# Optimization experiments

Measured on AMD Instinct MI355X. Metric: run time of the kernel, lower is better.

## Reference

```python
import jax, jax.numpy as jnp
import numpy as np

N_STATE = 1024
N_HEAD = 16
HEAD_DIM = N_STATE // N_HEAD


def setup_inputs() -> dict:
    key = jax.random.key(0)
    ks = jax.random.split(key, 8)
    s = 0.02
    return {
        "x": jax.random.normal(ks[0], (4, 1500, N_STATE), dtype=jnp.float32),
        "Wq": jax.random.normal(ks[1], (N_STATE, N_STATE), dtype=jnp.float32) * s,
        "bq": jnp.zeros((N_STATE,), dtype=jnp.float32),
        "Wk": jax.random.normal(ks[2], (N_STATE, N_STATE), dtype=jnp.float32) * s,
        "Wv": jax.random.normal(ks[3], (N_STATE, N_STATE), dtype=jnp.float32) * s,
        "bv": jnp.zeros((N_STATE,), dtype=jnp.float32),
        "Wo": jax.random.normal(ks[4], (N_STATE, N_STATE), dtype=jnp.float32) * s,
        "bo": jnp.zeros((N_STATE,), dtype=jnp.float32),
    }


def reference(x, Wq, bq, Wk, Wv, bv, Wo, bo):
    B, S, _ = x.shape
    scale = HEAD_DIM ** (-0.5)
    # projections (torch Linear: y = x @ W.T + b)
    q = x @ Wq.T + bq
    k = x @ Wk.T
    v = x @ Wv.T + bv
    # [B, H, S, D]
    q = q.reshape(B, S, N_HEAD, HEAD_DIM).transpose(0, 2, 1, 3)
    k = k.reshape(B, S, N_HEAD, HEAD_DIM).transpose(0, 2, 1, 3)
    v = v.reshape(B, S, N_HEAD, HEAD_DIM).transpose(0, 2, 1, 3)
    # scores scaled AFTER the matmul, as in the original (qk * qk_scale)
    qk = jnp.einsum("bhqd,bhkd->bhqk", q, k) * scale
    w = jax.nn.softmax(qk, axis=-1)
    wv = jnp.einsum("bhqk,bhkd->bhqd", w, v)
    wv = wv.transpose(0, 2, 1, 3).reshape(B, S, N_STATE)
    return wv @ Wo.T + bo
```

## Files before the change

kernel.cpp:

```cpp
#include <hip/hip_runtime.h>
#include <stdint.h>

#define S_LEN  1500
#define S_PAD  1536
#define BATCH  4
#define NSTATE 1024
#define NHEAD  16
#define HDIM   64
#define MROWS  6000
#define C1 0.180336879f

typedef __attribute__((ext_vector_type(8)))  short short8;
typedef __attribute__((ext_vector_type(4)))  float floatx4;
typedef __attribute__((ext_vector_type(16))) float floatx16;

__device__ __forceinline__ unsigned short f2bf(float f) {
  union { float f; unsigned int u; } v; v.f = f;
  unsigned int r = v.u + 0x7fffu + ((v.u >> 16) & 1u);
  return (unsigned short)(r >> 16);
}

__device__ __forceinline__ void gld_lds16(const void* g, void* l) {
  __builtin_amdgcn_global_load_lds(
      (const __attribute__((address_space(1))) void*)g,
      (__attribute__((address_space(3))) void*)l, 16, 0, 0);
}

__global__ __launch_bounds__(256) void cvt_all(
    const float* __restrict__ x,  const float* __restrict__ Wq,
    const float* __restrict__ Wk, const float* __restrict__ Wv,
    const float* __restrict__ Wo, unsigned short* __restrict__ dst)
{
  const size_t NX = (size_t)MROWS * NSTATE;
  size_t e = ((size_t)blockIdx.x * 256 + threadIdx.x) * 4;
  const float* src; size_t off;
  if (e < NX) { src = x; off = e; }
  else {
    size_t t = e - NX;
    int wsel = (int)(t >> 20);
    off = t & ((1u << 20) - 1);
    src = (wsel == 0) ? Wq : (wsel == 1) ? Wk : (wsel == 2) ? Wv : Wo;
  }
  float4 v = *(const float4*)(src + off);
  uint2 o;
  o.x = (unsigned int)f2bf(v.x) | ((unsigned int)f2bf(v.y) << 16);
  o.y = (unsigned int)f2bf(v.z) | ((unsigned int)f2bf(v.w) << 16);
  *(uint2*)(dst + e) = o;
}

__device__ __forceinline__ void gemm128_32(
    const unsigned short* __restrict__ X,
    const unsigned short* __restrict__ W,
    const float* __restrict__ bias,
    void* __restrict__ Yv,
    int m0, int n0, float oscale, int outmode)
{
  __shared__ unsigned short As[2][128 * 32];
  __shared__ unsigned short Bs[2][128 * 32];

  const int tid  = threadIdx.x;
  const int lane = tid & 63;
  const int wid  = tid >> 6;
  const int wm   = (wid & 1) * 64;
  const int wn   = (wid >> 1) * 64;
  const int l31  = lane & 31;
  const int lhi  = lane >> 5;
  const int fr   = (l31 >> 1) & 3;

  floatx16 acc[2][2];
#pragma unroll
  for (int i = 0; i < 2; ++i)
#pragma unroll
    for (int j = 0; j < 2; ++j)
      acc[i][j] = (floatx16)(0.f);

  const int srow = tid >> 2;
  const int logc = (lane & 3) ^ ((srow >> 1) & 3);

  const char* xrp[2];
  const char* wrp[2];
#pragma unroll
  for (int r = 0; r < 2; ++r) {
    int arow = m0 + r * 64 + srow;
    if (arow > MROWS - 1) arow = MROWS - 1;
    xrp[r] = (const char*)X + (size_t)arow * NSTATE * 2 + logc * 16;
    int brow = n0 + r * 64 + srow;
    wrp[r] = (const char*)W + (size_t)brow * NSTATE * 2 + logc * 16;
  }

  for (int k0 = 0; k0 < NSTATE; k0 += 64) {
    __syncthreads();
#pragma unroll
    for (int h = 0; h < 2; ++h) {
      int kb = (k0 + h * 32) * 2;
#pragma unroll
      for (int r = 0; r < 2; ++r) {
        gld_lds16(xrp[r] + kb, (char*)As[h] + r * 4096 + wid * 1024);
        gld_lds16(wrp[r] + kb, (char*)Bs[h] + r * 4096 + wid * 1024);
      }
    }
    __syncthreads();

#pragma unroll
    for (int h = 0; h < 2; ++h) {
      short8 af[2][2], bf[2][2];
#pragma unroll
      for (int mt = 0; mt < 2; ++mt)
#pragma unroll
        for (int kc = 0; kc < 2; ++kc) {
          int row  = wm + mt * 32 + l31;
          int phys = (kc * 2 + lhi) ^ fr;
          af[mt][kc] = *(const short8*)(As[h] + row * 32 + phys * 8);
        }
#pragma unroll
      for (int nt = 0; nt < 2; ++nt)
#pragma unroll
        for (int kc = 0; kc < 2; ++kc) {
          int row  = wn + nt * 32 + l31;
          int phys = (kc * 2 + lhi) ^ fr;
          bf[nt][kc] = *(const short8*)(Bs[h] + row * 32 + phys * 8);
        }
#pragma unroll
      for (int mt = 0; mt < 2; ++mt)
#pragma unroll
        for (int nt = 0; nt < 2; ++nt)
#pragma unroll
          for (int kc = 0; kc < 2; ++kc)
            acc[mt][nt] = __builtin_amdgcn_mfma_f32_32x32x16_bf16(
                af[mt][kc], bf[nt][kc], acc[mt][nt], 0, 0, 0);
    }
  }

  if (outmode == 2) {
    unsigned short* vt = (unsigned short*)Yv;
#pragma unroll
    for (int nt = 0; nt < 2; ++nt) {
      int ng = n0 + wn + nt * 32 + l31;
      float bias_v = bias[ng];
      int d  = ng & 63;
      int hh = ng >> 6;
#pragma unroll
      for (int mt = 0; mt < 2; ++mt)
#pragma unroll
        for (int rq = 0; rq < 4; ++rq) {
          int mgq = m0 + wm + mt * 32 + 8 * rq + 4 * lhi;
          if (mgq < MROWS) {
            int bb = mgq / 1500;
            int s0 = mgq - 1500 * bb;
            float v0 = acc[mt][nt][rq * 4 + 0] + bias_v;
            float v1 = acc[mt][nt][rq * 4 + 1] + bias_v;
            float v2 = acc[mt][nt][rq * 4 + 2] + bias_v;
            float v3 = acc[mt][nt][rq * 4 + 3] + bias_v;
            uint2 pk2;
            pk2.x = (unsigned int)f2bf(v0) | ((unsigned int)f2bf(v1) << 16);
            pk2.y = (unsigned int)f2bf(v2) | ((unsigned int)f2bf(v3) << 16);
            *(uint2*)&vt[(((size_t)bb * NHEAD + hh) * HDIM + d) * S_PAD + s0] = pk2;
          }
        }
    }
  } else {
#pragma unroll
    for (int nt = 0; nt < 2; ++nt) {
      int ng = n0 + wn + nt * 32 + l31;
      float bias_v = bias ? bias[ng] : 0.f;
#pragma unroll
      for (int mt = 0; mt < 2; ++mt)
#pragma unroll
        for (int r = 0; r < 16; ++r) {
          int mg = m0 + wm + mt * 32 + (r & 3) + 8 * (r >> 2) + 4 * lhi;
          if (mg < MROWS) {
            float val = (acc[mt][nt][r] + bias_v) * oscale;
            if (outmode == 1) ((float*)Yv)[(size_t)mg * NSTATE + ng] = val;
            else ((unsigned short*)Yv)[(size_t)mg * NSTATE + ng] = f2bf(val);
          }
        }
    }
  }
}

__global__ __launch_bounds__(256) void proj_qkv(
    const unsigned short* __restrict__ X,
    const unsigned short* __restrict__ Wq, const unsigned short* __restrict__ Wk,
    const unsigned short* __restrict__ Wv,
    const float* __restrict__ bq, const float* __restrict__ bv,
    unsigned short* __restrict__ q, unsigned short* __restrict__ k,
    unsigned short* __restrict__ vt)
{
  const int id  = blockIdx.x;
  const int sid = (id & 7) * 141 + (id >> 3);
  const int z   = sid / 376;
  const int rem = sid - z * 376;
  const int m0  = (rem >> 3) * 128;
  const int n0  = (rem & 7) * 128;

  if (z == 0)      gemm128_32(X, Wq, bq, q,  m0, n0, C1,  0);
  else if (z == 1) gemm128_32(X, Wk, (const float*)nullptr, k, m0, n0, 1.0f, 0);
  else             gemm128_32(X, Wv, bv, vt, m0, n0, 1.0f, 2);
}

__global__ __launch_bounds__(256) void proj_o(
    const unsigned short* __restrict__ X, const unsigned short* __restrict__ W,
    const float* __restrict__ bias, float* __restrict__ Y)
{
  const int id  = blockIdx.x;
  const int sid = (id & 7) * 47 + (id >> 3);
  gemm128_32(X, W, bias, Y, (sid >> 3) * 128, (sid & 7) * 128, 1.0f, 1);
}

#define NHALF 24

__global__ __launch_bounds__(256, 4) void attn32t(
    const unsigned short* __restrict__ Q, const unsigned short* __restrict__ K,
    const unsigned short* __restrict__ VT, unsigned short* __restrict__ O)
{
  __shared__ unsigned short SMEM[16384];
  unsigned short* Os = SMEM;

  const int tid  = threadIdx.x;
  const int lane = tid & 63;
  const int w    = tid >> 6;
  const int l31  = lane & 31;
  const int lhi  = lane >> 5;

  const int id  = blockIdx.x;
  const int sid = (id & 7) * 96 + (id >> 3);
  const int qt  = sid % 12;
  const int hb  = sid / 12;
  const int h   = hb & 15;
  const int b   = hb >> 4;

  const size_t base  = ((size_t)b * S_LEN) * NSTATE + h * HDIM;
  const size_t vbase = (((size_t)b * NHEAD + h) * HDIM) * S_PAD;

  const int srow8 = lane >> 3;
  const int sc3   = lane & 7;

  short8 qf[4];
  {
    int qrow = qt * 128 + w * 32 + l31;
    if (qrow > S_LEN - 1) qrow = S_LEN - 1;
    const unsigned short* qp = Q + base + (size_t)qrow * NSTATE;
#pragma unroll
    for (int c = 0; c < 4; ++c)
      qf[c] = *(const short8*)(qp + c * 16 + lhi * 8);
  }

  short8 ones8;
#pragma unroll
  for (int i = 0; i < 8; ++i) ones8[i] = (short)0x3F80;

  floatx16 oacc[2];
  oacc[0] = (floatx16)(0.f);
  oacc[1] = (floatx16)(0.f);
  floatx16 lacc = (floatx16)(0.f);

  auto stage_half = [&](int u, int bi) {
    char* kbase = (char*)SMEM + bi * 8192;
    char* vbase_l = (char*)SMEM + 16384 + bi * 8192;
#pragma unroll
    for (int qq = 0; qq < 2; ++qq) {
      int cg   = w * 2 + qq;
      int row  = cg * 8 + srow8;
      int logc = sc3 ^ (row & 7);
      int s = u * 64 + row; if (s > S_LEN - 1) s = S_LEN - 1;
      gld_lds16(&K[base + (size_t)s * NSTATE + logc * 8], kbase + cg * 1024);
    }
#pragma unroll
    for (int qq = 0; qq < 2; ++qq) {
      int cg   = w * 2 + qq;
      int d    = cg * 8 + srow8;
      int logc = sc3 ^ (d & 7);
      gld_lds16(&VT[vbase + (size_t)d * S_PAD + u * 64 + logc * 8],
                vbase_l + cg * 1024);
    }
  };

  stage_half(0, 0);
  __syncthreads();

  for (int u = 0; u < NHALF; ++u) {
    const int cur = u & 1;
    if (u < NHALF - 1) stage_half(u + 1, cur ^ 1);

    const unsigned short* Ks  = SMEM + cur * 4096;
    const unsigned short* Vts = SMEM + 8192 + cur * 4096;

#pragma unroll
    for (int kvt = 0; kvt < 2; ++kvt) {
      int row = kvt * 32 + l31;
      floatx16 sacc = (floatx16)(0.f);
      __builtin_amdgcn_s_setprio(1);
#pragma unroll
      for (int c = 0; c < 4; ++c) {
        int phys = (c * 2 + lhi) ^ (row & 7);
        short8 ak = *(const short8*)(Ks + row * 64 + phys * 8);
        sacc = __builtin_amdgcn_mfma_f32_32x32x16_bf16(ak, qf[c], sacc, 0, 0, 0);
      }
      __builtin_amdgcn_s_setprio(0);

      if (u == NHALF - 1) {
        if (kvt == 1) {
#pragma unroll
          for (int r = 0; r < 16; ++r) sacc[r] = -3.0e38f;
        } else {
#pragma unroll
          for (int r = 12; r < 16; ++r) sacc[r] = lhi ? -3.0e38f : sacc[r];
        }
      }

      unsigned int pk[8], ex[8];
#pragma unroll
      for (int i = 0; i < 8; ++i) {
        float plo = exp2f(sacc[2 * i]);
        float phi = exp2f(sacc[2 * i + 1]);
        unsigned int rr;
        asm("v_cvt_pk_bf16_f32 %0, %1, %2" : "=v"(rr) : "v"(plo), "v"(phi));
        pk[i] = rr;
      }
#pragma unroll
      for (int i = 0; i < 8; ++i)
        ex[i] = __shfl_xor((unsigned int)pk[i], 32, 64);

      int4 f0i, f1i;
      f0i.x = lhi ? ex[2] : pk[0];
      f0i.y = lhi ? ex[3] : pk[1];
      f0i.z = lhi ? pk[2] : ex[0];
      f0i.w = lhi ? pk[3] : ex[1];
      f1i.x = lhi ? ex[6] : pk[4];
      f1i.y = lhi ? ex[7] : pk[5];
      f1i.z = lhi ? pk[6] : ex[4];
      f1i.w = lhi ? pk[7] : ex[5];
      short8 f0 = *(short8*)&f0i;
      short8 f1 = *(short8*)&f1i;

      __builtin_amdgcn_s_setprio(1);
      lacc = __builtin_amdgcn_mfma_f32_32x32x16_bf16(ones8, f0, lacc, 0, 0, 0);
      lacc = __builtin_amdgcn_mfma_f32_32x32x16_bf16(ones8, f1, lacc, 0, 0, 0);

#pragma unroll
      for (int dt = 0; dt < 2; ++dt) {
        int d = dt * 32 + l31;
        int p0 = ((kvt * 4 + 0) + lhi) ^ (d & 7);
        int p1 = ((kvt * 4 + 2) + lhi) ^ (d & 7);
        short8 av0 = *(const short8*)(Vts + d * 64 + p0 * 8);
        short8 av1 = *(const short8*)(Vts + d * 64 + p1 * 8);
        oacc[dt] = __builtin_amdgcn_mfma_f32_32x32x16_bf16(av0, f0, oacc[dt], 0, 0, 0);
        oacc[dt] = __builtin_amdgcn_mfma_f32_32x32x16_bf16(av1, f1, oacc[dt], 0, 0, 0);
      }
      __builtin_amdgcn_s_setprio(0);
    }

    __syncthreads();
  }

  float inv = 1.f / lacc[0];

  __syncthreads();
#pragma unroll
  for (int dt = 0; dt < 2; ++dt)
#pragma unroll
    for (int g = 0; g < 4; ++g) {
      int d0 = dt * 32 + g * 8 + lhi * 4;
      float v0 = oacc[dt][4 * g + 0] * inv;
      float v1 = oacc[dt][4 * g + 1] * inv;
      float v2 = oacc[dt][4 * g + 2] * inv;
      float v3 = oacc[dt][4 * g + 3] * inv;
      uint2 pk2;
      pk2.x = (unsigned int)f2bf(v0) | ((unsigned int)f2bf(v1) << 16);
      pk2.y = (unsigned int)f2bf(v2) | ((unsigned int)f2bf(v3) << 16);
      *(uint2*)&Os[(w * 32 + l31) * 72 + d0] = pk2;
    }
  __syncthreads();
#pragma unroll
  for (int pass = 0; pass < 4; ++pass) {
    int e = pass * 256 + tid;
    int row = e >> 3, ch = e & 7;
    int s = qt * 128 + row;
    if (s < S_LEN)
      *(uint4*)&O[base + (size_t)s * NSTATE + ch * 8] = *(const uint4*)&Os[row * 72 + ch * 8];
  }
}

extern "C" void kernel_launch(void* const* d_in, const int* in_sizes, int n_in,
                              void* d_out, int out_size, void* d_ws, size_t ws_size,
                              hipStream_t stream) {
  const float* x  = (const float*)d_in[0];
  const float* Wq = (const float*)d_in[1];
  const float* bq = (const float*)d_in[2];
  const float* Wk = (const float*)d_in[3];
  const float* Wv = (const float*)d_in[4];
  const float* bv = (const float*)d_in[5];
  const float* Wo = (const float*)d_in[6];
  const float* bo = (const float*)d_in[7];
  float* out = (float*)d_out;

  const size_t NX  = (size_t)MROWS * NSTATE;
  const size_t NW  = (size_t)NSTATE * NSTATE;
  const size_t NVT = (size_t)BATCH * NHEAD * HDIM * S_PAD;

  unsigned short* xb  = (unsigned short*)d_ws;
  unsigned short* Wqb = xb  + NX;
  unsigned short* Wkb = Wqb + NW;
  unsigned short* Wvb = Wkb + NW;
  unsigned short* Wob = Wvb + NW;
  unsigned short* q   = Wob + NW;
  unsigned short* k   = q + NX;
  unsigned short* vt  = k + NX;
  unsigned short* wv  = xb;

  hipMemsetAsync(vt, 0, NVT * 2, stream);

  const size_t n4_total = (NX + 4 * NW) / 4;
  cvt_all<<<dim3((int)(n4_total / 256)), dim3(256), 0, stream>>>(x, Wq, Wk, Wv, Wo, xb);
  proj_qkv<<<dim3(1128), dim3(256), 0, stream>>>(xb, Wqb, Wkb, Wvb, bq, bv, q, k, vt);
  attn32t<<<dim3(768), dim3(256), 0, stream>>>(q, k, vt, wv);
  proj_o<<<dim3(376), dim3(256), 0, stream>>>(wv, Wob, bo, out);
}
```

Baseline: 256.1 us.

## Fuse V-pad zeroing into convert, swap V-proj MFMA operands, use permlane32 swap

Removes the full memset of the transposed V buffer and instead zeroes only the padded tail columns from extra blocks in the conversion kernel. The V projection swaps its MFMA operand order so each lane writes transposed V along the sequence dimension. The attention kernel precomputes K/V staging pointers and handles the last tile separately to avoid per-iteration clamping. It also replaces the eight cross-half shuffles with v_permlane32_swap. In exchange, the V projection now does scalar 2-byte stores and per-element bias loads, which may coalesce worse than the old packed stores.

```diff
diff --git a/kernel.cpp b/kernel.cpp
--- a/kernel.cpp
+++ b/kernel.cpp
@@ -29,10 +29,20 @@
 __global__ __launch_bounds__(256) void cvt_all(
     const float* __restrict__ x,  const float* __restrict__ Wq,
     const float* __restrict__ Wk, const float* __restrict__ Wv,
-    const float* __restrict__ Wo, unsigned short* __restrict__ dst)
+    const float* __restrict__ Wo, unsigned short* __restrict__ dst,
+    unsigned short* __restrict__ vt)
 {
-  const size_t NX = (size_t)MROWS * NSTATE;
+  const size_t NX   = (size_t)MROWS * NSTATE;
+  const size_t NTOT = NX + 4u * 1024u * 1024u;
   size_t e = ((size_t)blockIdx.x * 256 + threadIdx.x) * 4;
+  if (e >= NTOT) {
+    size_t p = (e - NTOT) >> 2;
+    int row = (int)(p / 9);
+    int off = (int)(p % 9) * 4;
+    uint2 z; z.x = 0u; z.y = 0u;
+    *(uint2*)&vt[(size_t)row * S_PAD + 1500 + off] = z;
+    return;
+  }
   const float* src; size_t off;
   if (e < NX) { src = x; off = e; }
   else {
@@ -120,42 +130,45 @@
           int phys = (kc * 2 + lhi) ^ fr;
           bf[nt][kc] = *(const short8*)(Bs[h] + row * 32 + phys * 8);
         }
-#pragma unroll
-      for (int mt = 0; mt < 2; ++mt)
-#pragma unroll
-        for (int nt = 0; nt < 2; ++nt)
-#pragma unroll
-          for (int kc = 0; kc < 2; ++kc)
-            acc[mt][nt] = __builtin_amdgcn_mfma_f32_32x32x16_bf16(
-                af[mt][kc], bf[nt][kc], acc[mt][nt], 0, 0, 0);
+      if (outmode == 2) {
+#pragma unroll
+        for (int mt = 0; mt < 2; ++mt)
+#pragma unroll
+          for (int nt = 0; nt < 2; ++nt)
+#pragma unroll
+            for (int kc = 0; kc < 2; ++kc)
+              acc[mt][nt] = __builtin_amdgcn_mfma_f32_32x32x16_bf16(
+                  bf[nt][kc], af[mt][kc], acc[mt][nt], 0, 0, 0);
+      } else {
+#pragma unroll
+        for (int mt = 0; mt < 2; ++mt)
+#pragma unroll
+          for (int nt = 0; nt < 2; ++nt)
+#pragma unroll
+            for (int kc = 0; kc < 2; ++kc)
+              acc[mt][nt] = __builtin_amdgcn_mfma_f32_32x32x16_bf16(
+                  af[mt][kc], bf[nt][kc], acc[mt][nt], 0, 0, 0);
+      }
     }
   }
 
   if (outmode == 2) {
     unsigned short* vt = (unsigned short*)Yv;
 #pragma unroll
-    for (int nt = 0; nt < 2; ++nt) {
-      int ng = n0 + wn + nt * 32 + l31;
-      float bias_v = bias[ng];
-      int d  = ng & 63;
-      int hh = ng >> 6;
-#pragma unroll
-      for (int mt = 0; mt < 2; ++mt)
-#pragma unroll
-        for (int rq = 0; rq < 4; ++rq) {
-          int mgq = m0 + wm + mt * 32 + 8 * rq + 4 * lhi;
-          if (mgq < MROWS) {
-            int bb = mgq / 1500;
-            int s0 = mgq - 1500 * bb;
-            float v0 = acc[mt][nt][rq * 4 + 0] + bias_v;
-            float v1 = acc[mt][nt][rq * 4 + 1] + bias_v;
-            float v2 = acc[mt][nt][rq * 4 + 2] + bias_v;
-            float v3 = acc[mt][nt][rq * 4 + 3] + bias_v;
-            uint2 pk2;
-            pk2.x = (unsigned int)f2bf(v0) | ((unsigned int)f2bf(v1) << 16);
-            pk2.y = (unsigned int)f2bf(v2) | ((unsigned int)f2bf(v3) << 16);
-            *(uint2*)&vt[(((size_t)bb * NHEAD + hh) * HDIM + d) * S_PAD + s0] = pk2;
-          }
+    for (int mt = 0; mt < 2; ++mt) {
+      int sg = m0 + wm + mt * 32 + l31;
+      bool ok = sg < MROWS;
+      int bb = sg / 1500;
+      int s0 = sg - bb * 1500;
+#pragma unroll
+      for (int nt = 0; nt < 2; ++nt)
+#pragma unroll
+        for (int r = 0; r < 16; ++r) {
+          int ng = n0 + wn + nt * 32 + (r & 3) + 8 * (r >> 2) + 4 * lhi;
+          float val = acc[mt][nt][r] + bias[ng];
+          if (ok)
+            vt[(((size_t)bb * NHEAD + (ng >> 6)) * HDIM + (ng & 63)) * S_PAD + s0] =
+                f2bf(val);
         }
     }
   } else {
@@ -234,6 +247,14 @@
 
   const int srow8 = lane >> 3;
   const int sc3   = lane & 7;
+  const int swc   = sc3 ^ srow8;
+
+  const char* kq0 = (const char*)K +
+      (base + (size_t)(w * 16 + srow8) * NSTATE + (size_t)swc * 8) * 2;
+  const char* kq1 = kq0 + (size_t)8 * NSTATE * 2;
+  const char* vq0 = (const char*)VT +
+      (vbase + (size_t)(w * 16 + srow8) * S_PAD + (size_t)swc * 8) * 2;
+  const char* vq1 = vq0 + (size_t)8 * S_PAD * 2;
 
   short8 qf[4];
   {
@@ -254,33 +275,38 @@
   oacc[1] = (floatx16)(0.f);
   floatx16 lacc = (floatx16)(0.f);
 
-  auto stage_half = [&](int u, int bi) {
-    char* kbase = (char*)SMEM + bi * 8192;
-    char* vbase_l = (char*)SMEM + 16384 + bi * 8192;
+  auto stageN = [&](int u, int bi) {
+    char* kb = (char*)SMEM + bi * 8192;
+    char* vb = (char*)SMEM + 16384 + bi * 8192;
+    size_t ko = (size_t)u * (64 * NSTATE * 2);
+    size_t vo = (size_t)u * (64 * 2);
+    gld_lds16(kq0 + ko, kb + (w * 2 + 0) * 1024);
+    gld_lds16(kq1 + ko, kb + (w * 2 + 1) * 1024);
+    gld_lds16(vq0 + vo, vb + (w * 2 + 0) * 1024);
+    gld_lds16(vq1 + vo, vb + (w * 2 + 1) * 1024);
+  };
+  auto stageC = [&](int bi) {
+    char* kb = (char*)SMEM + bi * 8192;
+    char* vb = (char*)SMEM + 16384 + bi * 8192;
 #pragma unroll
     for (int qq = 0; qq < 2; ++qq) {
-      int cg   = w * 2 + qq;
-      int row  = cg * 8 + srow8;
-      int logc = sc3 ^ (row & 7);
-      int s = u * 64 + row; if (s > S_LEN - 1) s = S_LEN - 1;
-      gld_lds16(&K[base + (size_t)s * NSTATE + logc * 8], kbase + cg * 1024);
-    }
-#pragma unroll
-    for (int qq = 0; qq < 2; ++qq) {
-      int cg   = w * 2 + qq;
-      int d    = cg * 8 + srow8;
-      int logc = sc3 ^ (d & 7);
-      gld_lds16(&VT[vbase + (size_t)d * S_PAD + u * 64 + logc * 8],
-                vbase_l + cg * 1024);
-    }
+      int s = 1472 + w * 16 + qq * 8 + srow8;
+      if (s > S_LEN - 1) s = S_LEN - 1;
+      gld_lds16((const char*)K + (base + (size_t)s * NSTATE + (size_t)swc * 8) * 2,
+                kb + (w * 2 + qq) * 1024);
+    }
+    size_t vo = (size_t)23 * (64 * 2);
+    gld_lds16(vq0 + vo, vb + (w * 2 + 0) * 1024);
+    gld_lds16(vq1 + vo, vb + (w * 2 + 1) * 1024);
   };
 
-  stage_half(0, 0);
+  stageN(0, 0);
   __syncthreads();
 
   for (int u = 0; u < NHALF; ++u) {
     const int cur = u & 1;
-    if (u < NHALF - 1) stage_half(u + 1, cur ^ 1);
+    if (u < NHALF - 2)       stageN(u + 1, cur ^ 1);
+    else if (u == NHALF - 2) stageC(cur ^ 1);
 
     const unsigned short* Ks  = SMEM + cur * 4096;
     const unsigned short* Vts = SMEM + 8192 + cur * 4096;
@@ -308,7 +334,7 @@
         }
       }
 
-      unsigned int pk[8], ex[8];
+      unsigned int pk[8];
 #pragma unroll
       for (int i = 0; i < 8; ++i) {
         float plo = exp2f(sacc[2 * i]);
@@ -317,19 +343,16 @@
         asm("v_cvt_pk_bf16_f32 %0, %1, %2" : "=v"(rr) : "v"(plo), "v"(phi));
         pk[i] = rr;
       }
-#pragma unroll
-      for (int i = 0; i < 8; ++i)
-        ex[i] = __shfl_xor((unsigned int)pk[i], 32, 64);
-
+
+      unsigned int a0 = pk[0], a1 = pk[1], b0 = pk[2], b1 = pk[3];
+      asm("v_permlane32_swap_b32 %0, %1" : "+v"(a0), "+v"(b0));
+      asm("v_permlane32_swap_b32 %0, %1" : "+v"(a1), "+v"(b1));
+      unsigned int c0 = pk[4], c1 = pk[5], d0 = pk[6], d1 = pk[7];
+      asm("v_permlane32_swap_b32 %0, %1" : "+v"(c0), "+v"(d0));
+      asm("v_permlane32_swap_b32 %0, %1" : "+v"(c1), "+v"(d1));
       int4 f0i, f1i;
-      f0i.x = lhi ? ex[2] : pk[0];
-      f0i.y = lhi ? ex[3] : pk[1];
-      f0i.z = lhi ? pk[2] : ex[0];
-      f0i.w = lhi ? pk[3] : ex[1];
-      f1i.x = lhi ? ex[6] : pk[4];
-      f1i.y = lhi ? ex[7] : pk[5];
-      f1i.z = lhi ? pk[6] : ex[4];
-      f1i.w = lhi ? pk[7] : ex[5];
+      f0i.x = a0; f0i.y = a1; f0i.z = b0; f0i.w = b1;
+      f1i.x = c0; f1i.y = c1; f1i.z = d0; f1i.w = d1;
       short8 f0 = *(short8*)&f0i;
       short8 f1 = *(short8*)&f1i;
 
@@ -396,7 +419,6 @@
 
   const size_t NX  = (size_t)MROWS * NSTATE;
   const size_t NW  = (size_t)NSTATE * NSTATE;
-  const size_t NVT = (size_t)BATCH * NHEAD * HDIM * S_PAD;
 
   unsigned short* xb  = (unsigned short*)d_ws;
   unsigned short* Wqb = xb  + NX;
@@ -408,10 +430,11 @@
   unsigned short* vt  = k + NX;
   unsigned short* wv  = xb;
 
-  hipMemsetAsync(vt, 0, NVT * 2, stream);
-
   const size_t n4_total = (NX + 4 * NW) / 4;
-  cvt_all<<<dim3((int)(n4_total / 256)), dim3(256), 0, stream>>>(x, Wq, Wk, Wv, Wo, xb);
+  const int main_blocks = (int)(n4_total / 256);
+  const int pad_blocks  = (BATCH * NHEAD * HDIM * 9) / 256;
+  cvt_all<<<dim3(main_blocks + pad_blocks), dim3(256), 0, stream>>>(
+      x, Wq, Wk, Wv, Wo, xb, vt);
   proj_qkv<<<dim3(1128), dim3(256), 0, stream>>>(xb, Wqb, Wkb, Wvb, bq, bv, q, k, vt);
   attn32t<<<dim3(768), dim3(256), 0, stream>>>(q, k, vt, wv);
   proj_o<<<dim3(376), dim3(256), 0, stream>>>(wv, Wob, bo, out);
```

Result: no change. 254.7 us (-0.5%).
